# Optimization experiments

Measured on AMD Instinct MI355X. Metric: run time of the kernel, lower is better.

## Reference

```python
import jax, jax.numpy as jnp
import numpy as np

N = 10000        # nodes
E = 320000       # edges (avg degree 32)
W = 256          # width (assert width >= 256)
H = 8            # num_head (RESCALE_EDGE assumed (1,1) -> nhead=8, dhead=32)
D = W // H       # per-head dim
BOND = 33        # EMBED_BOND[0]
BAG = 3          # indices per edge bag
EPS_GN = 1e-5


def setup_inputs() -> dict:
    key = jax.random.key(0)
    ks = jax.random.split(key, 12)
    x = jax.random.normal(ks[0], (N, W), dtype=jnp.float32)
    edge_idx = jax.random.randint(ks[1], (2, E), 0, N)
    edge_attr = jax.random.randint(ks[2], (E, BAG), 0, BOND)
    # node in-degree wrt scatter target edge_idx[1], clamped to >= 1
    deg = jax.ops.segment_sum(jnp.ones((E,), jnp.float32), edge_idx[1], num_segments=N)
    deg = jnp.maximum(deg, 1.0)
    s = 1.0 / np.sqrt(W)
    W_src = jax.random.normal(ks[3], (W, W), dtype=jnp.float32) * s
    W_tgt = jax.random.normal(ks[4], (W, W), dtype=jnp.float32) * s
    emb = jax.random.normal(ks[5], (BOND, W), dtype=jnp.float32) * 0.02
    emb = emb.at[0].set(0.0)  # padding_idx=0 row is zeros
    sd = 1.0 / np.sqrt(D)
    W_gate = jax.random.normal(ks[6], (H, D, D), dtype=jnp.float32) * sd  # grouped conv1d k=1
    W_val = jax.random.normal(ks[7], (H, D, D), dtype=jnp.float32) * sd
    W_post = jax.random.normal(ks[8], (W, W), dtype=jnp.float32) * s
    deg_param = jnp.zeros((W,), jnp.float32) - 0.01  # DegreeLayer degree_init
    return {"x": x, "deg": deg, "edge_idx": edge_idx, "edge_attr": edge_attr,
            "W_src": W_src, "W_tgt": W_tgt, "emb": emb,
            "W_gate": W_gate, "W_val": W_val, "W_post": W_post,
            "deg_param": deg_param}


def reference(x, deg, edge_idx, edge_attr, W_src, W_tgt, emb, W_gate, W_val, W_post, deg_param):
    # src/tgt 1x1 Conv1d == per-node linear, then edge gather
    xs = x @ W_src.T                      # [N, W]
    xt = x @ W_tgt.T                      # [N, W]
    xx = xs[edge_idx[0]] + xt[edge_idx[1]]  # [E, W]

    # EmbeddingBag(mode='mean', padding_idx=0): padded entries excluded
    mask = (edge_attr != 0).astype(xx.dtype)            # [E, BAG]
    bag = jnp.einsum('ebc,eb->ec', emb[edge_attr], mask)  # [E, W]
    cnt = jnp.maximum(mask.sum(-1, keepdims=True), 1.0)
    gate_bias = bag / cnt

    # GroupNorm(H, W, affine=False) over [E, W, 1]
    xg = xx.reshape(-1, H, D)
    mu = xg.mean(-1, keepdims=True)
    var = xg.var(-1, keepdims=True)
    xn = (xg - mu) / jnp.sqrt(var + EPS_GN)              # [E, H, D]

    # gated grouped 1x1 convs (dropout is identity at eval)
    gin = xn + gate_bias.reshape(-1, H, D)
    gate = jax.nn.relu(jnp.einsum('ehd,hfd->ehf', gin, W_gate))
    val = jnp.einsum('ehd,hfd->ehf', xn, W_val)
    act = (gate * val).reshape(-1, W)                    # [E, W]
    out_e = act @ W_post.T                               # [E, W]

    # scatter-sum to nodes, then degree rescale
    agg = jax.ops.segment_sum(out_e, edge_idx[1], num_segments=x.shape[0])
    return jnp.power(deg[:, None], deg_param) * agg      # [N, W]
```

## Files before the change

### kernel.cpp

```cpp
#include <hip/hip_runtime.h>

#define WID 256
#define EPS_GN 1e-5f

typedef __bf16 v8bf __attribute__((ext_vector_type(8)));
typedef __bf16 v2bf __attribute__((ext_vector_type(2)));
typedef float  v4f  __attribute__((ext_vector_type(4)));
typedef float  v2f  __attribute__((ext_vector_type(2)));

__device__ inline unsigned short f2b(float f) {
    unsigned int u = __builtin_bit_cast(unsigned int, f);
    unsigned int r = (u + 0x7fffu + ((u >> 16) & 1u)) >> 16;
    return (unsigned short)r;
}
__device__ inline float lo16(unsigned int u) { return __builtin_bit_cast(float, u << 16); }
__device__ inline float hi16(unsigned int u) { return __builtin_bit_cast(float, u & 0xffff0000u); }
__device__ inline v2f unpk(unsigned int u) {
    v2f r; r.x = lo16(u); r.y = hi16(u); return r;
}
#if __has_builtin(__builtin_elementwise_max)
__device__ inline v2f relu2(v2f a) { return __builtin_elementwise_max(a, (v2f){0.f, 0.f}); }
#else
__device__ inline v2f relu2(v2f a) { v2f r; r.x = fmaxf(a.x, 0.f); r.y = fmaxf(a.y, 0.f); return r; }
#endif

#if __has_builtin(__builtin_amdgcn_cvt_pk_bf16_f32)
__device__ inline unsigned int pkbf(float a, float b) {
    v2bf r = __builtin_amdgcn_cvt_pk_bf16_f32(a, b);
    return __builtin_bit_cast(unsigned int, r);
}
#else
__device__ inline unsigned int pkbf(float a, float b) {
    return (unsigned int)f2b(a) | ((unsigned int)f2b(b) << 16);
}
#endif

#if __has_builtin(__builtin_amdgcn_fdot2_f32_bf16)
__device__ inline float pairsum(unsigned int u, float s) {
    v2bf p = __builtin_bit_cast(v2bf, u);
    v2bf ones = __builtin_bit_cast(v2bf, 0x3f803f80u);
    return __builtin_amdgcn_fdot2_f32_bf16(p, ones, s, false);
}
#else
__device__ inline float pairsum(unsigned int u, float s) {
    return s + lo16(u) + hi16(u);
}
#endif

__global__ void cast_k(const float* __restrict__ Wsrc, const float* __restrict__ Wtgt,
                       const float* __restrict__ Wp, const float* __restrict__ Wg,
                       const float* __restrict__ Wv, const float* __restrict__ emb,
                       unsigned short* __restrict__ Wsb, unsigned short* __restrict__ Wtb,
                       unsigned short* __restrict__ Wpb, unsigned short* __restrict__ Wgb,
                       unsigned short* __restrict__ Wvb, unsigned short* __restrict__ embWgT,
                       int* __restrict__ cnt, int* __restrict__ ssrc,
                       int* __restrict__ stgt, int* __restrict__ sattr,
                       int N, int BOND, int E, int NT32) {
    int i = blockIdx.x * 256 + threadIdx.x;
    int gsz = gridDim.x * 256;
    for (int j = i; j < N; j += gsz) cnt[j] = 0;
    for (int j = E + i; j < NT32; j += gsz) { ssrc[j] = 0; stgt[j] = 0; sattr[j] = 0; }
    for (int j = i; j < 65536; j += gsz) {
        Wsb[j] = f2b(Wsrc[j]); Wtb[j] = f2b(Wtgt[j]); Wpb[j] = f2b(Wp[j]);
    }
    for (int j = i; j < 8192; j += gsz) { Wgb[j] = f2b(Wg[j]); Wvb[j] = f2b(Wv[j]); }
    for (int j = i; j < 8192; j += gsz) {
        int jr = j >> 5, k = j & 31;
        int kk = k ? k : 32;
        float sacc = 0.f;
        if (kk < BOND) {
            int h = jr >> 5, f = jr & 31;
            const float* er = emb + (size_t)kk * WID + h * 32;
            const float* wr = Wg + h * 1024 + f * 32;
#pragma unroll
            for (int d = 0; d < 32; d++) sacc += er[d] * wr[d];
        }
        embWgT[jr * 32 + k] = f2b(sacc);
    }
}

__global__ __launch_bounds__(256, 2)
void prepproj_k(const float* __restrict__ x, const unsigned short* __restrict__ Wsb,
                const unsigned short* __restrict__ Wtb, const int* __restrict__ eidx,
                unsigned short* __restrict__ xsb, unsigned short* __restrict__ xtb,
                int* __restrict__ cnt, float* __restrict__ aggact,
                int N, int E, int PB, int AUX) {
    __shared__ unsigned short ab[32 * 264];
    int t = threadIdx.x, b = blockIdx.x;

    if (b >= PB) {
        int atid = (b - PB) * 256 + t, asz = AUX * 256;
        {
            float4* ap = (float4*)aggact;
            int n4 = (N * WID) >> 2;
            for (int i = atid; i < n4; i += asz) ap[i] = make_float4(0.f, 0.f, 0.f, 0.f);
        }
        for (int i = atid; i < E; i += asz) atomicAdd(&cnt[eidx[E + i]], 1);
        return;
    }

    int n0 = b * 32;
#pragma unroll
    for (int ch = 0; ch < 8; ch++) {
        int flat = ch * 1024 + t * 4;
        int row = flat >> 8, col = flat & 255;
        int n = n0 + row;
        float4 v = (n < N) ? *(const float4*)&x[(size_t)n * WID + col]
                           : make_float4(0.f, 0.f, 0.f, 0.f);
        *(uint2*)&ab[row * 264 + col] = make_uint2(pkbf(v.x, v.y), pkbf(v.z, v.w));
    }
    __syncthreads();
    int w = t >> 6, lane = t & 63, m = lane & 15, kg = lane >> 4;
#pragma unroll
    for (int pass = 0; pass < 2; pass++) {
        const unsigned short* Wb = pass ? Wtb : Wsb;
        unsigned short* outp = pass ? xtb : xsb;
        v4f acc[2][4];
#pragma unroll
        for (int mt = 0; mt < 2; mt++)
#pragma unroll
            for (int nt = 0; nt < 4; nt++) acc[mt][nt] = (v4f){0.f, 0.f, 0.f, 0.f};
#pragma unroll
        for (int kt = 0; kt < 8; kt++) {
            int k0 = kt * 32 + kg * 8;
            v8bf a0 = *(const v8bf*)&ab[m * 264 + k0];
            v8bf a1 = *(const v8bf*)&ab[(16 + m) * 264 + k0];
#pragma unroll
            for (int nt = 0; nt < 4; nt++) {
                int j = w * 64 + nt * 16 + m;
                v8bf bfr = *(const v8bf*)&Wb[j * 256 + k0];
                acc[0][nt] = __builtin_amdgcn_mfma_f32_16x16x32_bf16(bfr, a0, acc[0][nt], 0, 0, 0);
                acc[1][nt] = __builtin_amdgcn_mfma_f32_16x16x32_bf16(bfr, a1, acc[1][nt], 0, 0, 0);
            }
        }
#pragma unroll
        for (int mt = 0; mt < 2; mt++) {
            int n = n0 + mt * 16 + m;
            if (n < N) {
#pragma unroll
                for (int nt = 0; nt < 4; nt++) {
                    int j0 = w * 64 + nt * 16 + kg * 4;
                    *(uint2*)&outp[(size_t)n * WID + j0] =
                        make_uint2(pkbf(acc[mt][nt][0], acc[mt][nt][1]),
                                   pkbf(acc[mt][nt][2], acc[mt][nt][3]));
                }
            }
        }
    }
}

__global__ void scan_k(const int* __restrict__ cnt, int* __restrict__ cur, int N) {
    __shared__ int buf[10240];
    __shared__ int part[1024];
    int t = threadIdx.x;
    int C = (N + 1023) >> 10;
    int M = C << 10;
    for (int i = t; i < M; i += 1024) buf[i] = (i < N) ? cnt[i] : 0;
    __syncthreads();
    int base0 = t * C;
    int s = 0;
    for (int i = 0; i < C; i++) s += buf[base0 + i];
    part[t] = s;
    __syncthreads();
    for (int d = 1; d < 1024; d <<= 1) {
        int v = (t >= d) ? part[t - d] : 0;
        __syncthreads();
        part[t] += v;
        __syncthreads();
    }
    int base = (t == 0) ? 0 : part[t - 1];
    for (int i = 0; i < C; i++) {
        int idx = base0 + i;
        int v = buf[idx];
        buf[idx] = base;
        base += v;
    }
    __syncthreads();
    for (int i = t; i < N; i += 1024) cur[i] = buf[i];
}

__global__ void scat_k(const int* __restrict__ eidx, const int* __restrict__ eattr,
                       int* __restrict__ cur, int* __restrict__ ssrc,
                       int* __restrict__ stgt, int* __restrict__ sattr, int E) {
    int i = blockIdx.x * 256 + threadIdx.x;
    if (i < E) {
        int tg = eidx[E + i];
        int p = atomicAdd(&cur[tg], 1);
        ssrc[p] = eidx[i];
        stgt[p] = tg;
        const int* ap = eattr + (size_t)i * 3;
        sattr[p] = (ap[0] & 63) | ((ap[1] & 63) << 6) | ((ap[2] & 63) << 12);
    }
}

__global__ __launch_bounds__(256, 8)
void edge_k(const unsigned short* __restrict__ xsb, const unsigned short* __restrict__ xtb,
            const int* __restrict__ ssrc, const int* __restrict__ stgt,
            const int* __restrict__ sattr, const unsigned short* __restrict__ Wgb,
            const unsigned short* __restrict__ Wvb, const unsigned short* __restrict__ embWgT,
            float* __restrict__ aggact, int E, int NT, int PER) {
    __shared__ unsigned short xxb[8704];
    __shared__ unsigned short Mld[32 * 40];
    __shared__ int src_s[32], tgt_s[32];
    __shared__ int segmask_s;

    int tile = (blockIdx.x & 7) * PER + (blockIdx.x >> 3);
    if (tile >= NT) return;
    int t = threadIdx.x;
    int e0 = tile * 32;
    int ne = min(32, E - e0);

    {
        int tgtv = -1;
        if (t < 32) {
            int e = e0 + t;
            src_s[t] = ssrc[e];
            int tg = stgt[e];
            tgt_s[t] = tg;
            int pa = sattr[e];
            uint4* Mr = (uint4*)&Mld[t * 40];
#pragma unroll
            for (int q = 0; q < 4; q++) Mr[q] = make_uint4(0u, 0u, 0u, 0u);
            int a0 = pa & 63, a1 = (pa >> 6) & 63, a2 = (pa >> 12) & 63;
            int c = (a0 != 0) + (a1 != 0) + (a2 != 0);
            float inv = (c > 0) ? 1.f / (float)c : 0.f;
            float wa = inv * (float)(1 + (a1 == a0) + (a2 == a0));
            float wb = inv * (float)(1 + (a2 == a1));
            if (a0) Mld[t * 40 + (a0 & 31)] = f2b(wa);
            if (a1 && a1 != a0) Mld[t * 40 + (a1 & 31)] = f2b(wb);
            if (a2 && a2 != a0 && a2 != a1) Mld[t * 40 + (a2 & 31)] = f2b(inv);
            tgtv = (t < ne) ? tg : -1;
        }
        if (t < 64) {
            int nxt = __shfl_down(tgtv, 1);
            bool flag = (t < ne) && ((t == ne - 1) || (nxt != tgtv));
            unsigned long long bal = __ballot(flag);
            if (t == 0) segmask_s = (int)(unsigned int)bal;
        }
    }
    __syncthreads();

    {
        int e = t >> 3, c = t & 7;
        int sn = src_s[e], g = tgt_s[e];
        const uint4* ps = (const uint4*)(xsb + (size_t)sn * WID);
        const uint4* pt = (const uint4*)(xtb + (size_t)g * WID);
        uint4 us[4], ut[4];
#pragma unroll
        for (int i = 0; i < 4; i++) { us[i] = ps[c + 8 * i]; ut[i] = pt[c + 8 * i]; }
        v2f v2[4][4];
        float sum[4], sq[4];
#pragma unroll
        for (int i = 0; i < 4; i++) {
            const unsigned int* au = (const unsigned int*)&us[i];
            const unsigned int* bu = (const unsigned int*)&ut[i];
            v2f s2 = (v2f){0.f, 0.f}, q2 = (v2f){0.f, 0.f};
#pragma unroll
            for (int q = 0; q < 4; q++) {
                v2f a = unpk(au[q]) + unpk(bu[q]);
                v2[i][q] = a;
                s2 += a;
                q2 += a * a;
            }
            sum[i] = s2.x + s2.y;
            sq[i]  = q2.x + q2.y;
        }
#pragma unroll
        for (int mask = 1; mask <= 2; mask <<= 1)
#pragma unroll
            for (int i = 0; i < 4; i++) {
                sum[i] += __shfl_xor(sum[i], mask);
                sq[i]  += __shfl_xor(sq[i], mask);
            }
#pragma unroll
        for (int i = 0; i < 4; i++) {
            float mu = sum[i] * (1.f / 32.f);
            float var = sq[i] * (1.f / 32.f) - mu * mu;
            float rs = rsqrtf(var + EPS_GN);
            float nmr = -mu * rs;
            v2f rs2 = (v2f){rs, rs}, nm2 = (v2f){nmr, nmr};
            unsigned int pk[4];
#pragma unroll
            for (int q = 0; q < 4; q++) {
                v2f r = v2[i][q] * rs2 + nm2;
                pk[q] = pkbf(r.x, r.y);
            }
            *(uint4*)&xxb[e * 264 + (c + 8 * i) * 8] = make_uint4(pk[0], pk[1], pk[2], pk[3]);
        }
    }
    __syncthreads();

    {
        int w = t >> 6, lane = t & 63, m = lane & 15, kg = lane >> 4;
        v8bf axn[2][2], aM[2];
#pragma unroll
        for (int mt = 0; mt < 2; mt++) {
            int row = mt * 16 + m;
            axn[0][mt] = *(const v8bf*)&xxb[row * 264 + (w * 2 + 0) * 32 + kg * 8];
            axn[1][mt] = *(const v8bf*)&xxb[row * 264 + (w * 2 + 1) * 32 + kg * 8];
            aM[mt] = *(const v8bf*)&Mld[row * 40 + kg * 8];
        }
        __syncthreads();
        v4f z = {0.f, 0.f, 0.f, 0.f};
#pragma unroll
        for (int hh = 0; hh < 2; hh++) {
            int h = w * 2 + hh;
#pragma unroll
            for (int nt = 0; nt < 2; nt++) {
                int fj = nt * 16 + m;
                int j = h * 32 + fj;
                v8bf bWg = *(const v8bf*)&Wgb[h * 1024 + fj * 32 + kg * 8];
                v8bf bWv = *(const v8bf*)&Wvb[h * 1024 + fj * 32 + kg * 8];
                v8bf bE  = *(const v8bf*)&embWgT[j * 32 + kg * 8];
#pragma unroll
                for (int mt = 0; mt < 2; mt++) {
                    v4f cgm = __builtin_amdgcn_mfma_f32_16x16x32_bf16(axn[hh][mt], bWg, z, 0, 0, 0);
                    cgm = __builtin_amdgcn_mfma_f32_16x16x32_bf16(aM[mt], bE, cgm, 0, 0, 0);
                    v4f cv = __builtin_amdgcn_mfma_f32_16x16x32_bf16(axn[hh][mt], bWv, z, 0, 0, 0);
                    v2f g0 = (v2f){cgm[0], cgm[1]}, g1 = (v2f){cgm[2], cgm[3]};
                    v2f h0 = (v2f){cv[0], cv[1]},  h1 = (v2f){cv[2], cv[3]};
                    g0 = relu2(g0) * h0;
                    g1 = relu2(g1) * h1;
                    int e0i = mt * 16 + kg * 4;
                    *(unsigned int*)&xxb[j * 34 + e0i]     = pkbf(g0.x, g0.y);
                    *(unsigned int*)&xxb[j * 34 + e0i + 2] = pkbf(g1.x, g1.y);
                }
            }
        }
    }
    __syncthreads();

    {
        unsigned int mask = (unsigned int)__builtin_amdgcn_readfirstlane(segmask_s);
        float sum = 0.f;
#pragma unroll
        for (int i = 0; i < 16; i++) {
            unsigned int r = *(const unsigned int*)&xxb[t * 34 + 2 * i];
            if (!((mask >> (2 * i)) & 1)) {
                sum = pairsum(r, sum);
                if ((mask >> (2 * i + 1)) & 1) {
                    int tg = __builtin_amdgcn_readfirstlane(tgt_s[2 * i + 1]);
                    atomicAdd(&aggact[(size_t)tg * WID + t], sum);
                    sum = 0.f;
                }
            } else {
                sum += lo16(r);
                int tg = __builtin_amdgcn_readfirstlane(tgt_s[2 * i]);
                atomicAdd(&aggact[(size_t)tg * WID + t], sum);
                sum = hi16(r);
                if ((mask >> (2 * i + 1)) & 1) {
                    int tg2 = __builtin_amdgcn_readfirstlane(tgt_s[2 * i + 1]);
                    atomicAdd(&aggact[(size_t)tg2 * WID + t], sum);
                    sum = 0.f;
                }
            }
        }
    }
}

__global__ __launch_bounds__(256, 2)
void post_k(const float* __restrict__ aggact, const unsigned short* __restrict__ Wpb,
            const float* __restrict__ deg, const float* __restrict__ dp,
            float* __restrict__ out, int N) {
    __shared__ unsigned short ab[32 * 264];
    __shared__ float degl[32];
    int t = threadIdx.x;
    int n0 = blockIdx.x * 32;
#pragma unroll
    for (int ch = 0; ch < 8; ch++) {
        int flat = ch * 1024 + t * 4;
        int row = flat >> 8, col = flat & 255;
        int n = n0 + row;
        float4 v = (n < N) ? *(const float4*)&aggact[(size_t)n * WID + col]
                           : make_float4(0.f, 0.f, 0.f, 0.f);
        *(uint2*)&ab[row * 264 + col] = make_uint2(pkbf(v.x, v.y), pkbf(v.z, v.w));
    }
    if (t < 32) {
        int n = n0 + t;
        degl[t] = (n < N) ? log2f(deg[n]) : 0.f;
    }
    __syncthreads();
    int w = t >> 6, lane = t & 63, m = lane & 15, kg = lane >> 4;
    v4f acc[2][4];
#pragma unroll
    for (int mt = 0; mt < 2; mt++)
#pragma unroll
        for (int nt = 0; nt < 4; nt++) acc[mt][nt] = (v4f){0.f, 0.f, 0.f, 0.f};
#pragma unroll
    for (int kt = 0; kt < 8; kt++) {
        int k0 = kt * 32 + kg * 8;
        v8bf a0 = *(const v8bf*)&ab[m * 264 + k0];
        v8bf a1 = *(const v8bf*)&ab[(16 + m) * 264 + k0];
#pragma unroll
        for (int nt = 0; nt < 4; nt++) {
            int j = w * 64 + nt * 16 + m;
            v8bf b = *(const v8bf*)&Wpb[j * 256 + k0];
            acc[0][nt] = __builtin_amdgcn_mfma_f32_16x16x32_bf16(b, a0, acc[0][nt], 0, 0, 0);
            acc[1][nt] = __builtin_amdgcn_mfma_f32_16x16x32_bf16(b, a1, acc[1][nt], 0, 0, 0);
        }
    }
#pragma unroll
    for (int mt = 0; mt < 2; mt++) {
        int n = n0 + mt * 16 + m;
        if (n < N) {
            float ld = degl[mt * 16 + m];
#pragma unroll
            for (int nt = 0; nt < 4; nt++) {
                int j0 = w * 64 + nt * 16 + kg * 4;
                float4 dv = *(const float4*)&dp[j0];
                float4 o;
                o.x = exp2f(dv.x * ld) * acc[mt][nt][0];
                o.y = exp2f(dv.y * ld) * acc[mt][nt][1];
                o.z = exp2f(dv.z * ld) * acc[mt][nt][2];
                o.w = exp2f(dv.w * ld) * acc[mt][nt][3];
                *(float4*)&out[(size_t)n * WID + j0] = o;
            }
        }
    }
}

extern "C" void kernel_launch(void* const* d_in, const int* in_sizes, int n_in,
                              void* d_out, int out_size, void* d_ws, size_t ws_size,
                              hipStream_t stream) {
    const float* x    = (const float*)d_in[0];
    const float* deg  = (const float*)d_in[1];
    const int*   eidx = (const int*)d_in[2];
    const int*   eatt = (const int*)d_in[3];
    const float* Wsrc = (const float*)d_in[4];
    const float* Wtgt = (const float*)d_in[5];
    const float* emb  = (const float*)d_in[6];
    const float* Wg   = (const float*)d_in[7];
    const float* Wv   = (const float*)d_in[8];
    const float* Wp   = (const float*)d_in[9];
    const float* dp   = (const float*)d_in[10];
    int N = in_sizes[0] / WID;
    int E = in_sizes[2] / 2;
    int BOND = in_sizes[6] / WID;

    int NT = (E + 31) / 32;
    int NT32 = NT * 32;

    float* ws     = (float*)d_ws;
    float* aggact = ws;
    int*   cnt    = (int*)(aggact + (size_t)N * WID);
    int*   cur    = cnt + N;
    int*   ssrc   = cur + N;
    int*   stgt   = ssrc + NT32;
    int*   sattr  = stgt + NT32;
    unsigned short* xsb = (unsigned short*)(sattr + NT32);
    unsigned short* xtb = xsb + (size_t)N * WID;
    unsigned short* Wsb = xtb + (size_t)N * WID;
    unsigned short* Wtb = Wsb + 65536;
    unsigned short* Wpb = Wtb + 65536;
    unsigned short* Wgb = Wpb + 65536;
    unsigned short* Wvb = Wgb + 8192;
    unsigned short* embWgT = Wvb + 8192;

    int PB = (N + 31) / 32;
    int AUX = 128;
    int PER = (NT + 7) / 8;

    cast_k<<<320, 256, 0, stream>>>(Wsrc, Wtgt, Wp, Wg, Wv, emb,
                                    Wsb, Wtb, Wpb, Wgb, Wvb, embWgT,
                                    cnt, ssrc, stgt, sattr, N, BOND, E, NT32);
    prepproj_k<<<PB + AUX, 256, 0, stream>>>(x, Wsb, Wtb, eidx, xsb, xtb, cnt, aggact,
                                             N, E, PB, AUX);
    scan_k<<<1, 1024, 0, stream>>>(cnt, cur, N);
    scat_k<<<(E + 255) / 256, 256, 0, stream>>>(eidx, eatt, cur, ssrc, stgt, sattr, E);
    edge_k<<<PER * 8, 256, 0, stream>>>(xsb, xtb, ssrc, stgt, sattr, Wgb, Wvb, embWgT,
                                        aggact, E, NT, PER);
    post_k<<<(N + 31) / 32, 256, 0, stream>>>(aggact, Wpb, deg, dp, (float*)d_out, N);
}
```

Before: 216.8 us.

## Split node projections into smaller blocks, move aggact zeroing, use packed FP32 asm

```diff
diff --git a/kernel.cpp b/kernel.cpp
--- a/kernel.cpp
+++ b/kernel.cpp
@@ -18,11 +18,16 @@
 __device__ inline v2f unpk(unsigned int u) {
     v2f r; r.x = lo16(u); r.y = hi16(u); return r;
 }
-#if __has_builtin(__builtin_elementwise_max)
-__device__ inline v2f relu2(v2f a) { return __builtin_elementwise_max(a, (v2f){0.f, 0.f}); }
-#else
-__device__ inline v2f relu2(v2f a) { v2f r; r.x = fmaxf(a.x, 0.f); r.y = fmaxf(a.y, 0.f); return r; }
-#endif
+
+__device__ inline v2f pk_add(v2f a, v2f b) {
+    v2f d; asm("v_pk_add_f32 %0, %1, %2" : "=v"(d) : "v"(a), "v"(b)); return d;
+}
+__device__ inline v2f pk_mul(v2f a, v2f b) {
+    v2f d; asm("v_pk_mul_f32 %0, %1, %2" : "=v"(d) : "v"(a), "v"(b)); return d;
+}
+__device__ inline v2f pk_fma(v2f a, v2f b, v2f c) {
+    v2f d; asm("v_pk_fma_f32 %0, %1, %2, %3" : "=v"(d) : "v"(a), "v"(b), "v"(c)); return d;
+}
 
 #if __has_builtin(__builtin_amdgcn_cvt_pk_bf16_f32)
 __device__ inline unsigned int pkbf(float a, float b) {
@@ -55,10 +60,16 @@
                        unsigned short* __restrict__ Wvb, unsigned short* __restrict__ embWgT,
                        int* __restrict__ cnt, int* __restrict__ ssrc,
                        int* __restrict__ stgt, int* __restrict__ sattr,
+                       float* __restrict__ aggact,
                        int N, int BOND, int E, int NT32) {
     int i = blockIdx.x * 256 + threadIdx.x;
     int gsz = gridDim.x * 256;
     for (int j = i; j < N; j += gsz) cnt[j] = 0;
+    {
+        float4* ap = (float4*)aggact;
+        int n4 = (N * WID) >> 2;
+        for (int j = i; j < n4; j += gsz) ap[j] = make_float4(0.f, 0.f, 0.f, 0.f);
+    }
     for (int j = E + i; j < NT32; j += gsz) { ssrc[j] = 0; stgt[j] = 0; sattr[j] = 0; }
     for (int j = i; j < 65536; j += gsz) {
         Wsb[j] = f2b(Wsrc[j]); Wtb[j] = f2b(Wtgt[j]); Wpb[j] = f2b(Wp[j]);
@@ -79,29 +90,27 @@
     }
 }
 
-__global__ __launch_bounds__(256, 2)
+__global__ __launch_bounds__(256, 6)
 void prepproj_k(const float* __restrict__ x, const unsigned short* __restrict__ Wsb,
                 const unsigned short* __restrict__ Wtb, const int* __restrict__ eidx,
                 unsigned short* __restrict__ xsb, unsigned short* __restrict__ xtb,
-                int* __restrict__ cnt, float* __restrict__ aggact,
-                int N, int E, int PB, int AUX) {
-    __shared__ unsigned short ab[32 * 264];
+                int* __restrict__ cnt, int N, int E, int PB2, int AUX) {
+    __shared__ unsigned short ab[16 * 264];
     int t = threadIdx.x, b = blockIdx.x;
 
-    if (b >= PB) {
-        int atid = (b - PB) * 256 + t, asz = AUX * 256;
-        {
-            float4* ap = (float4*)aggact;
-            int n4 = (N * WID) >> 2;
-            for (int i = atid; i < n4; i += asz) ap[i] = make_float4(0.f, 0.f, 0.f, 0.f);
-        }
+    if (b >= PB2) {
+        int atid = (b - PB2) * 256 + t, asz = AUX * 256;
         for (int i = atid; i < E; i += asz) atomicAdd(&cnt[eidx[E + i]], 1);
         return;
     }
 
-    int n0 = b * 32;
-#pragma unroll
-    for (int ch = 0; ch < 8; ch++) {
+    int pass = b & 1;
+    int n0 = (b >> 1) * 16;
+    const unsigned short* Wb = pass ? Wtb : Wsb;
+    unsigned short* outp = pass ? xtb : xsb;
+
+#pragma unroll
+    for (int ch = 0; ch < 4; ch++) {
         int flat = ch * 1024 + t * 4;
         int row = flat >> 8, col = flat & 255;
         int n = n0 + row;
@@ -111,40 +120,28 @@
     }
     __syncthreads();
     int w = t >> 6, lane = t & 63, m = lane & 15, kg = lane >> 4;
-#pragma unroll
-    for (int pass = 0; pass < 2; pass++) {
-        const unsigned short* Wb = pass ? Wtb : Wsb;
-        unsigned short* outp = pass ? xtb : xsb;
-        v4f acc[2][4];
-#pragma unroll
-        for (int mt = 0; mt < 2; mt++)
-#pragma unroll
-            for (int nt = 0; nt < 4; nt++) acc[mt][nt] = (v4f){0.f, 0.f, 0.f, 0.f};
-#pragma unroll
-        for (int kt = 0; kt < 8; kt++) {
-            int k0 = kt * 32 + kg * 8;
-            v8bf a0 = *(const v8bf*)&ab[m * 264 + k0];
-            v8bf a1 = *(const v8bf*)&ab[(16 + m) * 264 + k0];
-#pragma unroll
-            for (int nt = 0; nt < 4; nt++) {
-                int j = w * 64 + nt * 16 + m;
-                v8bf bfr = *(const v8bf*)&Wb[j * 256 + k0];
-                acc[0][nt] = __builtin_amdgcn_mfma_f32_16x16x32_bf16(bfr, a0, acc[0][nt], 0, 0, 0);
-                acc[1][nt] = __builtin_amdgcn_mfma_f32_16x16x32_bf16(bfr, a1, acc[1][nt], 0, 0, 0);
-            }
-        }
-#pragma unroll
-        for (int mt = 0; mt < 2; mt++) {
-            int n = n0 + mt * 16 + m;
-            if (n < N) {
-#pragma unroll
-                for (int nt = 0; nt < 4; nt++) {
-                    int j0 = w * 64 + nt * 16 + kg * 4;
-                    *(uint2*)&outp[(size_t)n * WID + j0] =
-                        make_uint2(pkbf(acc[mt][nt][0], acc[mt][nt][1]),
-                                   pkbf(acc[mt][nt][2], acc[mt][nt][3]));
-                }
-            }
+    v4f acc[4];
+#pragma unroll
+    for (int nt = 0; nt < 4; nt++) acc[nt] = (v4f){0.f, 0.f, 0.f, 0.f};
+#pragma unroll
+    for (int kt = 0; kt < 8; kt++) {
+        int k0 = kt * 32 + kg * 8;
+        v8bf a0 = *(const v8bf*)&ab[m * 264 + k0];
+#pragma unroll
+        for (int nt = 0; nt < 4; nt++) {
+            int j = w * 64 + nt * 16 + m;
+            v8bf bfr = *(const v8bf*)&Wb[j * 256 + k0];
+            acc[nt] = __builtin_amdgcn_mfma_f32_16x16x32_bf16(bfr, a0, acc[nt], 0, 0, 0);
+        }
+    }
+    int n = n0 + m;
+    if (n < N) {
+#pragma unroll
+        for (int nt = 0; nt < 4; nt++) {
+            int j0 = w * 64 + nt * 16 + kg * 4;
+            *(uint2*)&outp[(size_t)n * WID + j0] =
+                make_uint2(pkbf(acc[nt][0], acc[nt][1]),
+                           pkbf(acc[nt][2], acc[nt][3]));
         }
     }
 }
@@ -257,10 +254,10 @@
             v2f s2 = (v2f){0.f, 0.f}, q2 = (v2f){0.f, 0.f};
 #pragma unroll
             for (int q = 0; q < 4; q++) {
-                v2f a = unpk(au[q]) + unpk(bu[q]);
+                v2f a = pk_add(unpk(au[q]), unpk(bu[q]));
                 v2[i][q] = a;
-                s2 += a;
-                q2 += a * a;
+                s2 = pk_add(s2, a);
+                q2 = pk_fma(a, a, q2);
             }
             sum[i] = s2.x + s2.y;
             sq[i]  = q2.x + q2.y;
@@ -282,7 +279,7 @@
             unsigned int pk[4];
 #pragma unroll
             for (int q = 0; q < 4; q++) {
-                v2f r = v2[i][q] * rs2 + nm2;
+                v2f r = pk_fma(v2[i][q], rs2, nm2);
                 pk[q] = pkbf(r.x, r.y);
             }
             *(uint4*)&xxb[e * 264 + (c + 8 * i) * 8] = make_uint4(pk[0], pk[1], pk[2], pk[3]);
@@ -317,10 +314,10 @@
                     v4f cgm = __builtin_amdgcn_mfma_f32_16x16x32_bf16(axn[hh][mt], bWg, z, 0, 0, 0);
                     cgm = __builtin_amdgcn_mfma_f32_16x16x32_bf16(aM[mt], bE, cgm, 0, 0, 0);
                     v4f cv = __builtin_amdgcn_mfma_f32_16x16x32_bf16(axn[hh][mt], bWv, z, 0, 0, 0);
-                    v2f g0 = (v2f){cgm[0], cgm[1]}, g1 = (v2f){cgm[2], cgm[3]};
-                    v2f h0 = (v2f){cv[0], cv[1]},  h1 = (v2f){cv[2], cv[3]};
-                    g0 = relu2(g0) * h0;
-                    g1 = relu2(g1) * h1;
+                    v2f g0 = (v2f){fmaxf(cgm[0], 0.f), fmaxf(cgm[1], 0.f)};
+                    v2f g1 = (v2f){fmaxf(cgm[2], 0.f), fmaxf(cgm[3], 0.f)};
+                    g0 = pk_mul(g0, (v2f){cv[0], cv[1]});
+                    g1 = pk_mul(g1, (v2f){cv[2], cv[3]});
                     int e0i = mt * 16 + kg * 4;
                     *(unsigned int*)&xxb[j * 34 + e0i]     = pkbf(g0.x, g0.y);
                     *(unsigned int*)&xxb[j * 34 + e0i + 2] = pkbf(g1.x, g1.y);
@@ -358,16 +355,16 @@
     }
 }
 
-__global__ __launch_bounds__(256, 2)
+__global__ __launch_bounds__(256, 6)
 void post_k(const float* __restrict__ aggact, const unsigned short* __restrict__ Wpb,
             const float* __restrict__ deg, const float* __restrict__ dp,
             float* __restrict__ out, int N) {
-    __shared__ unsigned short ab[32 * 264];
-    __shared__ float degl[32];
+    __shared__ unsigned short ab[16 * 264];
+    __shared__ float degl[16];
     int t = threadIdx.x;
-    int n0 = blockIdx.x * 32;
-#pragma unroll
-    for (int ch = 0; ch < 8; ch++) {
+    int n0 = blockIdx.x * 16;
+#pragma unroll
+    for (int ch = 0; ch < 4; ch++) {
         int flat = ch * 1024 + t * 4;
         int row = flat >> 8, col = flat & 255;
         int n = n0 + row;
@@ -375,46 +372,39 @@
                            : make_float4(0.f, 0.f, 0.f, 0.f);
         *(uint2*)&ab[row * 264 + col] = make_uint2(pkbf(v.x, v.y), pkbf(v.z, v.w));
     }
-    if (t < 32) {
+    if (t < 16) {
         int n = n0 + t;
         degl[t] = (n < N) ? log2f(deg[n]) : 0.f;
     }
     __syncthreads();
     int w = t >> 6, lane = t & 63, m = lane & 15, kg = lane >> 4;
-    v4f acc[2][4];
-#pragma unroll
-    for (int mt = 0; mt < 2; mt++)
-#pragma unroll
-        for (int nt = 0; nt < 4; nt++) acc[mt][nt] = (v4f){0.f, 0.f, 0.f, 0.f};
+    v4f acc[4];
+#pragma unroll
+    for (int nt = 0; nt < 4; nt++) acc[nt] = (v4f){0.f, 0.f, 0.f, 0.f};
 #pragma unroll
     for (int kt = 0; kt < 8; kt++) {
         int k0 = kt * 32 + kg * 8;
         v8bf a0 = *(const v8bf*)&ab[m * 264 + k0];
-        v8bf a1 = *(const v8bf*)&ab[(16 + m) * 264 + k0];
 #pragma unroll
         for (int nt = 0; nt < 4; nt++) {
             int j = w * 64 + nt * 16 + m;
             v8bf b = *(const v8bf*)&Wpb[j * 256 + k0];
-            acc[0][nt] = __builtin_amdgcn_mfma_f32_16x16x32_bf16(b, a0, acc[0][nt], 0, 0, 0);
-            acc[1][nt] = __builtin_amdgcn_mfma_f32_16x16x32_bf16(b, a1, acc[1][nt], 0, 0, 0);
-        }
-    }
-#pragma unroll
-    for (int mt = 0; mt < 2; mt++) {
-        int n = n0 + mt * 16 + m;
-        if (n < N) {
-            float ld = degl[mt * 16 + m];
-#pragma unroll
-            for (int nt = 0; nt < 4; nt++) {
-                int j0 = w * 64 + nt * 16 + kg * 4;
-                float4 dv = *(const float4*)&dp[j0];
-                float4 o;
-                o.x = exp2f(dv.x * ld) * acc[mt][nt][0];
-                o.y = exp2f(dv.y * ld) * acc[mt][nt][1];
-                o.z = exp2f(dv.z * ld) * acc[mt][nt][2];
-                o.w = exp2f(dv.w * ld) * acc[mt][nt][3];
-                *(float4*)&out[(size_t)n * WID + j0] = o;
-            }
+            acc[nt] = __builtin_amdgcn_mfma_f32_16x16x32_bf16(b, a0, acc[nt], 0, 0, 0);
+        }
+    }
+    int n = n0 + m;
+    if (n < N) {
+        float ld = degl[m];
+#pragma unroll
+        for (int nt = 0; nt < 4; nt++) {
+            int j0 = w * 64 + nt * 16 + kg * 4;
+            float4 dv = *(const float4*)&dp[j0];
+            float4 o;
+            o.x = exp2f(dv.x * ld) * acc[nt][0];
+            o.y = exp2f(dv.y * ld) * acc[nt][1];
+            o.z = exp2f(dv.z * ld) * acc[nt][2];
+            o.w = exp2f(dv.w * ld) * acc[nt][3];
+            *(float4*)&out[(size_t)n * WID + j0] = o;
         }
     }
 }
@@ -456,18 +446,19 @@
     unsigned short* Wvb = Wgb + 8192;
     unsigned short* embWgT = Wvb + 8192;
 
-    int PB = (N + 31) / 32;
+    int PB16 = (N + 15) / 16;
+    int PB2 = 2 * PB16;
     int AUX = 128;
     int PER = (NT + 7) / 8;
 
     cast_k<<<320, 256, 0, stream>>>(Wsrc, Wtgt, Wp, Wg, Wv, emb,
                                     Wsb, Wtb, Wpb, Wgb, Wvb, embWgT,
-                                    cnt, ssrc, stgt, sattr, N, BOND, E, NT32);
-    prepproj_k<<<PB + AUX, 256, 0, stream>>>(x, Wsb, Wtb, eidx, xsb, xtb, cnt, aggact,
-                                             N, E, PB, AUX);
+                                    cnt, ssrc, stgt, sattr, aggact, N, BOND, E, NT32);
+    prepproj_k<<<PB2 + AUX, 256, 0, stream>>>(x, Wsb, Wtb, eidx, xsb, xtb, cnt,
+                                              N, E, PB2, AUX);
     scan_k<<<1, 1024, 0, stream>>>(cnt, cur, N);
     scat_k<<<(E + 255) / 256, 256, 0, stream>>>(eidx, eatt, cur, ssrc, stgt, sattr, E);
     edge_k<<<PER * 8, 256, 0, stream>>>(xsb, xtb, ssrc, stgt, sattr, Wgb, Wvb, embWgT,
                                         aggact, E, NT, PER);
-    post_k<<<(N + 31) / 32, 256, 0, stream>>>(aggact, Wpb, deg, dp, (float*)d_out, N);
-}
+    post_k<<<PB16, 256, 0, stream>>>(aggact, Wpb, deg, dp, (float*)d_out, N);
+}
```

Measured after the change: 223.6 us. +3.1%, slower.

## Use packed f32 inline asm in edge kernel and raise occupancy bounds

Applied to the files above, without the earlier changes.

```diff
diff --git a/kernel.cpp b/kernel.cpp
--- a/kernel.cpp
+++ b/kernel.cpp
@@ -18,11 +18,16 @@
 __device__ inline v2f unpk(unsigned int u) {
     v2f r; r.x = lo16(u); r.y = hi16(u); return r;
 }
-#if __has_builtin(__builtin_elementwise_max)
-__device__ inline v2f relu2(v2f a) { return __builtin_elementwise_max(a, (v2f){0.f, 0.f}); }
-#else
-__device__ inline v2f relu2(v2f a) { v2f r; r.x = fmaxf(a.x, 0.f); r.y = fmaxf(a.y, 0.f); return r; }
-#endif
+
+__device__ inline v2f pk_add(v2f a, v2f b) {
+    v2f d; asm("v_pk_add_f32 %0, %1, %2" : "=v"(d) : "v"(a), "v"(b)); return d;
+}
+__device__ inline v2f pk_mul(v2f a, v2f b) {
+    v2f d; asm("v_pk_mul_f32 %0, %1, %2" : "=v"(d) : "v"(a), "v"(b)); return d;
+}
+__device__ inline v2f pk_fma(v2f a, v2f b, v2f c) {
+    v2f d; asm("v_pk_fma_f32 %0, %1, %2, %3" : "=v"(d) : "v"(a), "v"(b), "v"(c)); return d;
+}
 
 #if __has_builtin(__builtin_amdgcn_cvt_pk_bf16_f32)
 __device__ inline unsigned int pkbf(float a, float b) {
@@ -79,7 +84,7 @@
     }
 }
 
-__global__ __launch_bounds__(256, 2)
+__global__ __launch_bounds__(256, 3)
 void prepproj_k(const float* __restrict__ x, const unsigned short* __restrict__ Wsb,
                 const unsigned short* __restrict__ Wtb, const int* __restrict__ eidx,
                 unsigned short* __restrict__ xsb, unsigned short* __restrict__ xtb,
@@ -257,10 +262,10 @@
             v2f s2 = (v2f){0.f, 0.f}, q2 = (v2f){0.f, 0.f};
 #pragma unroll
             for (int q = 0; q < 4; q++) {
-                v2f a = unpk(au[q]) + unpk(bu[q]);
+                v2f a = pk_add(unpk(au[q]), unpk(bu[q]));
                 v2[i][q] = a;
-                s2 += a;
-                q2 += a * a;
+                s2 = pk_add(s2, a);
+                q2 = pk_fma(a, a, q2);
             }
             sum[i] = s2.x + s2.y;
             sq[i]  = q2.x + q2.y;
@@ -282,7 +287,7 @@
             unsigned int pk[4];
 #pragma unroll
             for (int q = 0; q < 4; q++) {
-                v2f r = v2[i][q] * rs2 + nm2;
+                v2f r = pk_fma(v2[i][q], rs2, nm2);
                 pk[q] = pkbf(r.x, r.y);
             }
             *(uint4*)&xxb[e * 264 + (c + 8 * i) * 8] = make_uint4(pk[0], pk[1], pk[2], pk[3]);
@@ -317,10 +322,10 @@
                     v4f cgm = __builtin_amdgcn_mfma_f32_16x16x32_bf16(axn[hh][mt], bWg, z, 0, 0, 0);
                     cgm = __builtin_amdgcn_mfma_f32_16x16x32_bf16(aM[mt], bE, cgm, 0, 0, 0);
                     v4f cv = __builtin_amdgcn_mfma_f32_16x16x32_bf16(axn[hh][mt], bWv, z, 0, 0, 0);
-                    v2f g0 = (v2f){cgm[0], cgm[1]}, g1 = (v2f){cgm[2], cgm[3]};
-                    v2f h0 = (v2f){cv[0], cv[1]},  h1 = (v2f){cv[2], cv[3]};
-                    g0 = relu2(g0) * h0;
-                    g1 = relu2(g1) * h1;
+                    v2f g0 = (v2f){fmaxf(cgm[0], 0.f), fmaxf(cgm[1], 0.f)};
+                    v2f g1 = (v2f){fmaxf(cgm[2], 0.f), fmaxf(cgm[3], 0.f)};
+                    g0 = pk_mul(g0, (v2f){cv[0], cv[1]});
+                    g1 = pk_mul(g1, (v2f){cv[2], cv[3]});
                     int e0i = mt * 16 + kg * 4;
                     *(unsigned int*)&xxb[j * 34 + e0i]     = pkbf(g0.x, g0.y);
                     *(unsigned int*)&xxb[j * 34 + e0i + 2] = pkbf(g1.x, g1.y);
@@ -358,7 +363,7 @@
     }
 }
 
-__global__ __launch_bounds__(256, 2)
+__global__ __launch_bounds__(256, 3)
 void post_k(const float* __restrict__ aggact, const unsigned short* __restrict__ Wpb,
             const float* __restrict__ deg, const float* __restrict__ dp,
             float* __restrict__ out, int N) {
@@ -469,5 +474,5 @@
     scat_k<<<(E + 255) / 256, 256, 0, stream>>>(eidx, eatt, cur, ssrc, stgt, sattr, E);
     edge_k<<<PER * 8, 256, 0, stream>>>(xsb, xtb, ssrc, stgt, sattr, Wgb, Wvb, embWgT,
                                         aggact, E, NT, PER);
-    post_k<<<(N + 31) / 32, 256, 0, stream>>>(aggact, Wpb, deg, dp, (float*)d_out, N);
-}
+    post_k<<<PB, 256, 0, stream>>>(aggact, Wpb, deg, dp, (float*)d_out, N);
+}
```

Result: no change. 219.7 us (+1.3%).
